# Kernel optimization log

Measured on AMD Instinct MI355X. Metric: run time of the kernel, lower is better.

The kernel has to match this reference:

```python
import jax, jax.numpy as jnp
import numpy as np

N, B, CIN = 2048, 16, 1
M = 4096
COUT = 64
R = 128


def setup_inputs() -> dict:
    key = jax.random.key(0)
    k1, k2, k3, k4, k5 = jax.random.split(key, 5)
    return {
        "context_in": jax.random.normal(k1, (N, B, CIN), dtype=jnp.float32),
        "context_out": jax.random.normal(k2, (N, B, COUT), dtype=jnp.float32),
        "target_in": jax.random.normal(k3, (M, B, CIN), dtype=jnp.float32),
        "lengthscale": jnp.ones((1,), dtype=jnp.float32),
        "W": jax.random.normal(k4, (R, COUT + 1), dtype=jnp.float32),
        "b": jax.random.normal(k5, (R,), dtype=jnp.float32),
    }


def reference(context_in, context_out, target_in, lengthscale, W, b):
    # context_in: (N,B,Cin), context_out: (N,B,Cout), target_in: (M,B,Cin)
    n, batch, _ = context_in.shape
    # density channel prepended -> (N,B,Cout+1)
    dens = jnp.ones((n, batch, 1), dtype=context_in.dtype)
    co = jnp.concatenate([dens, context_out], axis=-1)
    ci = jnp.transpose(context_in, (1, 0, 2))   # (B,N,Cin)
    ti = jnp.transpose(target_in, (1, 0, 2))    # (B,M,Cin)
    # squared pairwise distances (B,N,M)
    d2 = (jnp.sum(ci * ci, -1)[:, :, None]
          + jnp.sum(ti * ti, -1)[:, None, :]
          - 2.0 * jnp.einsum('bnd,bmd->bnm', ci, ti))
    d2 = jnp.maximum(d2, 0.0)
    # RBF kernel: exp(-0.5 * d2 / lengthscale^2)
    K = jnp.exp(-0.5 * d2 / (lengthscale[0] ** 2))  # (B,N,M)
    # weighted sum over context points: (B,M,Cout+1)
    out = jnp.einsum('nbc,bnm->bmc', co, K)
    # density normalization of non-density channels
    out = jnp.concatenate([out[..., :1], out[..., 1:] / (out[..., :1] + 1e-8)], axis=-1)
    # linear projection (Cout+1 -> R)
    out = out @ W.T + b
    return jnp.transpose(out, (1, 0, 2))  # (M,B,R)
```

## Files before the change

### kernel.cpp

```cpp
#include <hip/hip_runtime.h>
#include <hip/hip_bf16.h>


#define N_CTX 2048
#define BATCH 16
#define M_TGT 4096
#define COUT  64
#define RDIM  128

#define WS_COW_OFF  0u
#define WS_FB_OFF   0x400000u
#define WS_G_OFF    0xC00000u
#define WS_GD_OFF   0xC40000u
#define WS_WT_OFF   0xC41000u

#define SSCALE 0.8493222f

typedef __attribute__((ext_vector_type(8)))  short        bf16x8;
typedef __attribute__((ext_vector_type(4)))  float        floatx4;
typedef __attribute__((ext_vector_type(4)))  unsigned int uint4v;

#if __has_builtin(__builtin_amdgcn_exp2f)
#define EXP2F __builtin_amdgcn_exp2f
#else
#define EXP2F exp2f
#endif

__constant__ float RSQ[64] = {
    0.0f,        1.0f,        0.70710678f, 0.57735027f, 0.5f,        0.44721360f,
    0.40824829f, 0.37796447f, 0.35355339f, 0.33333333f, 0.31622777f, 0.30151134f,
    0.28867513f, 0.27735010f, 0.26726124f, 0.25819889f, 0.25f,       0.24253563f,
    0.23570226f, 0.22941573f, 0.22360680f, 0.21821789f, 0.21320072f, 0.20851441f,
    0.20412415f, 0.2f,        0.19611614f, 0.19245009f, 0.18898224f, 0.18569534f,
    0.18257419f, 0.17960530f, 0.17677670f, 0.17407766f, 0.17149859f, 0.16903085f,
    0.16666667f, 0.16439899f, 0.16222142f, 0.16012815f, 0.15811388f, 0.15617376f,
    0.15430335f, 0.15249857f, 0.15075567f, 0.14907120f, 0.14744196f, 0.14586499f,
    0.14433757f, 0.14285714f, 0.14142136f, 0.14002801f, 0.13867505f, 0.13736056f,
    0.13608276f, 0.13483997f, 0.13363062f, 0.13245324f, 0.13130643f, 0.13018891f,
    0.12909944f, 0.12803688f, 0.12700013f, 0.12598816f };

static __device__ __forceinline__ unsigned int packrn(float a, float b) {
    __hip_bfloat162 h = __float22bfloat162_rn(make_float2(a, b));
    return *reinterpret_cast<unsigned int*>(&h);
}
static __device__ __forceinline__ unsigned short f2bfs(float f) {
    __hip_bfloat16 h = __float2bfloat16(f);
    return *reinterpret_cast<unsigned short*>(&h);
}

__global__ __launch_bounds__(256)
void convdeepset_prep(const float* __restrict__ co, const float* __restrict__ W,
                      unsigned char* __restrict__ ws)
{
    unsigned short* cow = (unsigned short*)(ws + WS_COW_OFF);
    unsigned short* wt  = (unsigned short*)(ws + WS_WT_OFF);
    const int blk = blockIdx.x, tid = threadIdx.x;

    if (blk < 1024) {
        const int g    = blk * 4 + (tid >> 6);
        const int bb   = g & 15;
        const int nblk = g >> 4;
        const int c    = tid & 63;
        const float* rp = co + ((size_t)nblk * 8 * BATCH + bb) * COUT + c;
        unsigned int u[4];
#pragma unroll
        for (int j = 0; j < 4; ++j) {
            const float f0 = rp[(size_t)(2 * j)     * BATCH * COUT];
            const float f1 = rp[(size_t)(2 * j + 1) * BATCH * COUT];
            u[j] = packrn(f0, f1);
        }
        *(uint4v*)&cow[(size_t)bb * 131072 + nblk * 512 + c * 8] = *(uint4v*)u;
    } else {
        for (int f = tid; f < 8192; f += 256) {
            const int cp = f & 7, r = (f >> 3) & 127, ch = f >> 10;
            wt[ch * 1024 + r * 8 + cp] = f2bfs(W[r * 65 + 1 + ch * 8 + cp]);
        }
    }
}

__global__ __launch_bounds__(256)
void convdeepset_feat(const float* __restrict__ ci, const float* __restrict__ ls,
                      unsigned char* __restrict__ ws)
{
    float* fb = (float*)(ws + WS_FB_OFF);
    const int f = blockIdx.x * 256 + threadIdx.x;
    const int n = f & 2047, bb = f >> 11;
    const float w  = ci[(size_t)n * BATCH + bb] / ls[0];
    const float sy = SSCALE * w;
    float v = EXP2F(-sy * sy);
    float* o = fb + (size_t)bb * 64 * 2048 + n;
    o[0] = v;
#pragma unroll
    for (int k = 1; k < 64; ++k) {
        v *= w * RSQ[k];
        o[(size_t)k * 2048] = v;
    }
}

__global__ __launch_bounds__(256)
void convdeepset_g(unsigned char* __restrict__ ws)
{
    __shared__ float sred[4][64][16];
    __shared__ float sdens[4][16];
    const unsigned short* cow = (const unsigned short*)(ws + WS_COW_OFF);
    const float* fb = (const float*)(ws + WS_FB_OFF);
    float* G  = (float*)(ws + WS_G_OFF);
    float* gd = (float*)(ws + WS_GD_OFF);

    const int b  = blockIdx.x >> 2, kt = blockIdx.x & 3;
    const int tid = threadIdx.x, lane = tid & 63, wv = tid >> 6;
    const int g2 = lane >> 4, l15 = lane & 15;

    const float* ap = fb + ((size_t)b * 64 + kt * 16 + l15) * 2048
                    + wv * 512 + g2 * 8;
    const unsigned short* bp = cow + (size_t)b * 131072
                             + ((size_t)(wv * 16) * 4 + g2) * 512 + l15 * 8;

    floatx4 acc[4];
#pragma unroll
    for (int ct = 0; ct < 4; ++ct)
#pragma unroll
        for (int e = 0; e < 4; ++e) acc[ct][e] = 0.0f;
    float dpart = 0.0f;

#pragma unroll 4
    for (int s = 0; s < 16; ++s) {
        const floatx4 a0 = *(const floatx4*)(ap);
        const floatx4 a1 = *(const floatx4*)(ap + 4);
        ap += 32;
        const bf16x8 c0 = *(const bf16x8*)(bp);
        const bf16x8 c1 = *(const bf16x8*)(bp + 128);
        const bf16x8 c2 = *(const bf16x8*)(bp + 256);
        const bf16x8 c3 = *(const bf16x8*)(bp + 384);
        bp += 2048;
        dpart += a0.x + a0.y + a0.z + a0.w + a1.x + a1.y + a1.z + a1.w;
        const float fl[8] = {a0.x, a0.y, a0.z, a0.w, a1.x, a1.y, a1.z, a1.w};
        uint4v hw, lw;
#pragma unroll
        for (int p = 0; p < 4; ++p) {
            const unsigned int h = packrn(fl[2 * p], fl[2 * p + 1]);
            const float e0 = __builtin_bit_cast(float, h << 16);
            const float e1 = __builtin_bit_cast(float, h & 0xffff0000u);
            hw[p] = h;
            lw[p] = packrn(fl[2 * p] - e0, fl[2 * p + 1] - e1);
        }
        const bf16x8 ah = __builtin_bit_cast(bf16x8, hw);
        const bf16x8 al = __builtin_bit_cast(bf16x8, lw);
        acc[0] = __builtin_amdgcn_mfma_f32_16x16x32_bf16(ah, c0, acc[0], 0, 0, 0);
        acc[0] = __builtin_amdgcn_mfma_f32_16x16x32_bf16(al, c0, acc[0], 0, 0, 0);
        acc[1] = __builtin_amdgcn_mfma_f32_16x16x32_bf16(ah, c1, acc[1], 0, 0, 0);
        acc[1] = __builtin_amdgcn_mfma_f32_16x16x32_bf16(al, c1, acc[1], 0, 0, 0);
        acc[2] = __builtin_amdgcn_mfma_f32_16x16x32_bf16(ah, c2, acc[2], 0, 0, 0);
        acc[2] = __builtin_amdgcn_mfma_f32_16x16x32_bf16(al, c2, acc[2], 0, 0, 0);
        acc[3] = __builtin_amdgcn_mfma_f32_16x16x32_bf16(ah, c3, acc[3], 0, 0, 0);
        acc[3] = __builtin_amdgcn_mfma_f32_16x16x32_bf16(al, c3, acc[3], 0, 0, 0);
    }

    dpart += __shfl_xor(dpart, 16);
    dpart += __shfl_xor(dpart, 32);
    if (lane < 16) sdens[wv][lane] = dpart;
#pragma unroll
    for (int ct = 0; ct < 4; ++ct)
#pragma unroll
        for (int reg = 0; reg < 4; ++reg)
            sred[wv][lane][ct * 4 + reg] = acc[ct][reg];
    __syncthreads();

    {
        const int ct = tid >> 6, ln = tid & 63;
        const int c  = ct * 16 + (ln & 15);
#pragma unroll
        for (int reg = 0; reg < 4; ++reg) {
            const float ssum = sred[0][ln][ct * 4 + reg] + sred[1][ln][ct * 4 + reg]
                             + sred[2][ln][ct * 4 + reg] + sred[3][ln][ct * 4 + reg];
            const int k = (ln >> 4) * 4 + reg;
            G[((size_t)b * 64 + kt * 16 + k) * 64 + c] = ssum;
        }
    }
    if (tid < 16)
        gd[b * 64 + kt * 16 + tid]
            = sdens[0][tid] + sdens[1][tid] + sdens[2][tid] + sdens[3][tid];
}

__global__ __launch_bounds__(256)
void convdeepset_main(const float* __restrict__ ti, const float* __restrict__ ls,
                      const float* __restrict__ W,  const float* __restrict__ bias,
                      const unsigned char* __restrict__ ws, float* __restrict__ out)
{
    __shared__ float gsm[4096];
    __shared__ float gdl[64];
    __shared__ unsigned short vstage[4][1024];

    const int tid  = threadIdx.x;
    const int lane = tid & 63;
    const int wv   = tid >> 6;
    const int g2   = lane >> 4;
    const int l15  = lane & 15;

    const int b  = blockIdx.x & 15;
    const int mt = blockIdx.x >> 4;
    const int m0 = mt * 64 + wv * 16;

    const float* Gg = (const float*)(ws + WS_G_OFF) + (size_t)b * 4096;
#pragma unroll
    for (int j = 0; j < 4; ++j)
        ((float4*)gsm)[tid + j * 256] = ((const float4*)Gg)[tid + j * 256];
    if (tid < 64) gdl[tid] = ((const float*)(ws + WS_GD_OFF))[b * 64 + tid];
    __syncthreads();

    const float w  = ti[(size_t)(m0 + l15) * BATCH + b] / ls[0];
    const float sy = SSCALE * w;
    float f = EXP2F(-sy * sy);
    float dens = f * gdl[0];
    float fs[16];
#pragma unroll
    for (int j = 0; j < 16; ++j) fs[j] = 0.0f;
    if (g2 == 0) fs[0] = f;
#pragma unroll
    for (int k = 1; k < 64; ++k) {
        f *= w * RSQ[k];
        dens += f * gdl[k];
        if (((k >> 3) & 3) == g2) fs[((k >> 5) << 3) | (k & 7)] = f;
    }

    uint4v hw0, lw0, hw1, lw1;
#pragma unroll
    for (int p = 0; p < 4; ++p) {
        {
            const unsigned int h = packrn(fs[2 * p], fs[2 * p + 1]);
            const float e0 = __builtin_bit_cast(float, h << 16);
            const float e1 = __builtin_bit_cast(float, h & 0xffff0000u);
            hw0[p] = h;
            lw0[p] = packrn(fs[2 * p] - e0, fs[2 * p + 1] - e1);
        }
        {
            const unsigned int h = packrn(fs[8 + 2 * p], fs[8 + 2 * p + 1]);
            const float e0 = __builtin_bit_cast(float, h << 16);
            const float e1 = __builtin_bit_cast(float, h & 0xffff0000u);
            hw1[p] = h;
            lw1[p] = packrn(fs[8 + 2 * p] - e0, fs[8 + 2 * p + 1] - e1);
        }
    }
    const bf16x8 ah0 = __builtin_bit_cast(bf16x8, hw0);
    const bf16x8 al0 = __builtin_bit_cast(bf16x8, lw0);
    const bf16x8 ah1 = __builtin_bit_cast(bf16x8, hw1);
    const bf16x8 al1 = __builtin_bit_cast(bf16x8, lw1);

    floatx4 acc[4];
#pragma unroll
    for (int ct = 0; ct < 4; ++ct)
#pragma unroll
        for (int e = 0; e < 4; ++e) acc[ct][e] = 0.0f;
#pragma unroll
    for (int ct = 0; ct < 4; ++ct) {
#pragma unroll
        for (int wdw = 0; wdw < 2; ++wdw) {
            float gv[8];
#pragma unroll
            for (int j = 0; j < 8; ++j)
                gv[j] = gsm[(wdw * 32 + g2 * 8 + j) * 64 + ct * 16 + l15];
            uint4v gh, gl;
#pragma unroll
            for (int p = 0; p < 4; ++p) {
                const unsigned int h = packrn(gv[2 * p], gv[2 * p + 1]);
                const float e0 = __builtin_bit_cast(float, h << 16);
                const float e1 = __builtin_bit_cast(float, h & 0xffff0000u);
                gh[p] = h;
                gl[p] = packrn(gv[2 * p] - e0, gv[2 * p + 1] - e1);
            }
            const bf16x8 ghv = __builtin_bit_cast(bf16x8, gh);
            const bf16x8 glv = __builtin_bit_cast(bf16x8, gl);
            const bf16x8 ah = wdw ? ah1 : ah0;
            const bf16x8 al = wdw ? al1 : al0;
            acc[ct] = __builtin_amdgcn_mfma_f32_16x16x32_bf16(ah, ghv, acc[ct], 0, 0, 0);
            acc[ct] = __builtin_amdgcn_mfma_f32_16x16x32_bf16(al, ghv, acc[ct], 0, 0, 0);
            acc[ct] = __builtin_amdgcn_mfma_f32_16x16x32_bf16(ah, glv, acc[ct], 0, 0, 0);
        }
    }

    const unsigned short* wtg = (const unsigned short*)(ws + WS_WT_OFF);
    float dt[4], ffv[4];
#pragma unroll
    for (int reg = 0; reg < 4; ++reg) {
        const int m = (lane >> 4) * 4 + reg;
        dt[reg]  = __shfl(dens, m, 64);
        ffv[reg] = 1.0f / (fmaxf(dt[reg], 0.0f) + 1e-8f);
    }
    unsigned short* vs = vstage[wv];
#pragma unroll
    for (int reg = 0; reg < 4; ++reg) {
        const int m = (lane >> 4) * 4 + reg;
#pragma unroll
        for (int q = 0; q < 4; ++q) {
            const int c = q * 16 + l15;
            vs[(c >> 3) * 128 + m * 8 + (c & 7)] = f2bfs(acc[q][reg]);
        }
    }
    floatx4 pacc[8];
#pragma unroll
    for (int rt = 0; rt < 8; ++rt)
#pragma unroll
        for (int e = 0; e < 4; ++e) pacc[rt][e] = 0.0f;
#pragma unroll
    for (int s2 = 0; s2 < 2; ++s2) {
        const int ch = s2 * 4 + g2;
        const bf16x8 avp = *(const bf16x8*)&vs[ch * 128 + l15 * 8];
#pragma unroll
        for (int rt = 0; rt < 8; ++rt) {
            const bf16x8 bvp = *(const bf16x8*)&wtg[ch * 1024 + (rt * 16 + l15) * 8];
            pacc[rt] = __builtin_amdgcn_mfma_f32_16x16x32_bf16(avp, bvp, pacc[rt], 0, 0, 0);
        }
    }
#pragma unroll
    for (int rt = 0; rt < 8; ++rt) {
        const int r = rt * 16 + l15;
        const float w0v = W[r * 65];
        const float bv  = bias[r];
#pragma unroll
        for (int reg = 0; reg < 4; ++reg) {
            const int m = (lane >> 4) * 4 + reg;
            out[((size_t)(m0 + m) * BATCH + b) * RDIM + r]
                = pacc[rt][reg] * ffv[reg] + dt[reg] * w0v + bv;
        }
    }
}

extern "C" void kernel_launch(void* const* d_in, const int* in_sizes, int n_in,
                              void* d_out, int out_size, void* d_ws, size_t ws_size,
                              hipStream_t stream) {
    const float* ci   = (const float*)d_in[0];
    const float* co   = (const float*)d_in[1];
    const float* ti   = (const float*)d_in[2];
    const float* ls   = (const float*)d_in[3];
    const float* W    = (const float*)d_in[4];
    const float* bias = (const float*)d_in[5];
    float* o = (float*)d_out;
    (void)in_sizes; (void)n_in; (void)out_size; (void)ws_size;

    unsigned char* ws = (unsigned char*)d_ws;
    convdeepset_prep<<<1025, 256, 0, stream>>>(co, W, ws);
    convdeepset_feat<<<128, 256, 0, stream>>>(ci, ls, ws);
    convdeepset_g<<<64, 256, 0, stream>>>(ws);
    convdeepset_main<<<1024, 256, 0, stream>>>(ti, ls, W, bias, ws, o);
}
```

Baseline: 108.8 us.

## Merge feature kernel into prep and process two target tiles per block

The feature-basis computation moves into the prep kernel as an extra block range, removing one kernel launch. The main kernel now handles 128 targets per block instead of 64 and runs on half as many blocks. It splits G into hi/lo bf16 fragments once and reuses them for both tiles, so the G shared-memory load and conversion cost is spread over more targets. The cost is higher register pressure from the precomputed fragments and two feature sets, and fewer blocks to hide latency.

After: 107.5 us (median of 2 runs). Within noise of the previous version (-1.2%).

```diff
diff --git a/kernel.cpp b/kernel.cpp
--- a/kernel.cpp
+++ b/kernel.cpp
@@ -49,14 +49,14 @@
 }
 
 __global__ __launch_bounds__(256)
-void convdeepset_prep(const float* __restrict__ co, const float* __restrict__ W,
+void convdeepset_prep(const float* __restrict__ ci, const float* __restrict__ co,
+                      const float* __restrict__ ls, const float* __restrict__ W,
                       unsigned char* __restrict__ ws)
 {
-    unsigned short* cow = (unsigned short*)(ws + WS_COW_OFF);
-    unsigned short* wt  = (unsigned short*)(ws + WS_WT_OFF);
     const int blk = blockIdx.x, tid = threadIdx.x;
 
     if (blk < 1024) {
+        unsigned short* cow = (unsigned short*)(ws + WS_COW_OFF);
         const int g    = blk * 4 + (tid >> 6);
         const int bb   = g & 15;
         const int nblk = g >> 4;
@@ -70,30 +70,26 @@
             u[j] = packrn(f0, f1);
         }
         *(uint4v*)&cow[(size_t)bb * 131072 + nblk * 512 + c * 8] = *(uint4v*)u;
+    } else if (blk < 1152) {
+        float* fbp = (float*)(ws + WS_FB_OFF);
+        const int f = (blk - 1024) * 256 + tid;
+        const int n = f & 2047, bb = f >> 11;
+        const float w  = ci[(size_t)n * BATCH + bb] / ls[0];
+        const float sy = SSCALE * w;
+        float v = EXP2F(-sy * sy);
+        float* o = fbp + (size_t)bb * 64 * 2048 + n;
+        o[0] = v;
+#pragma unroll
+        for (int k = 1; k < 64; ++k) {
+            v *= w * RSQ[k];
+            o[(size_t)k * 2048] = v;
+        }
     } else {
+        unsigned short* wt = (unsigned short*)(ws + WS_WT_OFF);
         for (int f = tid; f < 8192; f += 256) {
             const int cp = f & 7, r = (f >> 3) & 127, ch = f >> 10;
             wt[ch * 1024 + r * 8 + cp] = f2bfs(W[r * 65 + 1 + ch * 8 + cp]);
         }
-    }
-}
-
-__global__ __launch_bounds__(256)
-void convdeepset_feat(const float* __restrict__ ci, const float* __restrict__ ls,
-                      unsigned char* __restrict__ ws)
-{
-    float* fb = (float*)(ws + WS_FB_OFF);
-    const int f = blockIdx.x * 256 + threadIdx.x;
-    const int n = f & 2047, bb = f >> 11;
-    const float w  = ci[(size_t)n * BATCH + bb] / ls[0];
-    const float sy = SSCALE * w;
-    float v = EXP2F(-sy * sy);
-    float* o = fb + (size_t)bb * 64 * 2048 + n;
-    o[0] = v;
-#pragma unroll
-    for (int k = 1; k < 64; ++k) {
-        v *= w * RSQ[k];
-        o[(size_t)k * 2048] = v;
     }
 }
 
@@ -199,7 +195,7 @@
 
     const int b  = blockIdx.x & 15;
     const int mt = blockIdx.x >> 4;
-    const int m0 = mt * 64 + wv * 16;
+    const int m0 = mt * 128 + wv * 16;
 
     const float* Gg = (const float*)(ws + WS_G_OFF) + (size_t)b * 4096;
 #pragma unroll
@@ -208,51 +204,9 @@
     if (tid < 64) gdl[tid] = ((const float*)(ws + WS_GD_OFF))[b * 64 + tid];
     __syncthreads();
 
-    const float w  = ti[(size_t)(m0 + l15) * BATCH + b] / ls[0];
-    const float sy = SSCALE * w;
-    float f = EXP2F(-sy * sy);
-    float dens = f * gdl[0];
-    float fs[16];
-#pragma unroll
-    for (int j = 0; j < 16; ++j) fs[j] = 0.0f;
-    if (g2 == 0) fs[0] = f;
-#pragma unroll
-    for (int k = 1; k < 64; ++k) {
-        f *= w * RSQ[k];
-        dens += f * gdl[k];
-        if (((k >> 3) & 3) == g2) fs[((k >> 5) << 3) | (k & 7)] = f;
-    }
-
-    uint4v hw0, lw0, hw1, lw1;
-#pragma unroll
-    for (int p = 0; p < 4; ++p) {
-        {
-            const unsigned int h = packrn(fs[2 * p], fs[2 * p + 1]);
-            const float e0 = __builtin_bit_cast(float, h << 16);
-            const float e1 = __builtin_bit_cast(float, h & 0xffff0000u);
-            hw0[p] = h;
-            lw0[p] = packrn(fs[2 * p] - e0, fs[2 * p + 1] - e1);
-        }
-        {
-            const unsigned int h = packrn(fs[8 + 2 * p], fs[8 + 2 * p + 1]);
-            const float e0 = __builtin_bit_cast(float, h << 16);
-            const float e1 = __builtin_bit_cast(float, h & 0xffff0000u);
-            hw1[p] = h;
-            lw1[p] = packrn(fs[8 + 2 * p] - e0, fs[8 + 2 * p + 1] - e1);
-        }
-    }
-    const bf16x8 ah0 = __builtin_bit_cast(bf16x8, hw0);
-    const bf16x8 al0 = __builtin_bit_cast(bf16x8, lw0);
-    const bf16x8 ah1 = __builtin_bit_cast(bf16x8, hw1);
-    const bf16x8 al1 = __builtin_bit_cast(bf16x8, lw1);
-
-    floatx4 acc[4];
+    bf16x8 ghv[4][2], glv[4][2];
 #pragma unroll
     for (int ct = 0; ct < 4; ++ct)
-#pragma unroll
-        for (int e = 0; e < 4; ++e) acc[ct][e] = 0.0f;
-#pragma unroll
-    for (int ct = 0; ct < 4; ++ct) {
 #pragma unroll
         for (int wdw = 0; wdw < 2; ++wdw) {
             float gv[8];
@@ -268,61 +222,122 @@
                 gh[p] = h;
                 gl[p] = packrn(gv[2 * p] - e0, gv[2 * p + 1] - e1);
             }
-            const bf16x8 ghv = __builtin_bit_cast(bf16x8, gh);
-            const bf16x8 glv = __builtin_bit_cast(bf16x8, gl);
-            const bf16x8 ah = wdw ? ah1 : ah0;
-            const bf16x8 al = wdw ? al1 : al0;
-            acc[ct] = __builtin_amdgcn_mfma_f32_16x16x32_bf16(ah, ghv, acc[ct], 0, 0, 0);
-            acc[ct] = __builtin_amdgcn_mfma_f32_16x16x32_bf16(al, ghv, acc[ct], 0, 0, 0);
-            acc[ct] = __builtin_amdgcn_mfma_f32_16x16x32_bf16(ah, glv, acc[ct], 0, 0, 0);
+            ghv[ct][wdw] = __builtin_bit_cast(bf16x8, gh);
+            glv[ct][wdw] = __builtin_bit_cast(bf16x8, gl);
+        }
+
+    const float wa = ti[(size_t)(m0 + l15) * BATCH + b] / ls[0];
+    const float wb = ti[(size_t)(m0 + 64 + l15) * BATCH + b] / ls[0];
+    const float sa = SSCALE * wa, sb = SSCALE * wb;
+    float fa  = EXP2F(-sa * sa);
+    float fb_ = EXP2F(-sb * sb);
+    float densa = fa * gdl[0], densb = fb_ * gdl[0];
+    float fsa[16], fsb[16];
+#pragma unroll
+    for (int j = 0; j < 16; ++j) { fsa[j] = 0.0f; fsb[j] = 0.0f; }
+    if (g2 == 0) { fsa[0] = fa; fsb[0] = fb_; }
+#pragma unroll
+    for (int k = 1; k < 64; ++k) {
+        fa  *= wa * RSQ[k];
+        fb_ *= wb * RSQ[k];
+        densa += fa  * gdl[k];
+        densb += fb_ * gdl[k];
+        if (((k >> 3) & 3) == g2) {
+            const int slot = ((k >> 5) << 3) | (k & 7);
+            fsa[slot] = fa;
+            fsb[slot] = fb_;
         }
     }
 
     const unsigned short* wtg = (const unsigned short*)(ws + WS_WT_OFF);
-    float dt[4], ffv[4];
-#pragma unroll
-    for (int reg = 0; reg < 4; ++reg) {
-        const int m = (lane >> 4) * 4 + reg;
-        dt[reg]  = __shfl(dens, m, 64);
-        ffv[reg] = 1.0f / (fmaxf(dt[reg], 0.0f) + 1e-8f);
-    }
-    unsigned short* vs = vstage[wv];
-#pragma unroll
-    for (int reg = 0; reg < 4; ++reg) {
-        const int m = (lane >> 4) * 4 + reg;
-#pragma unroll
-        for (int q = 0; q < 4; ++q) {
-            const int c = q * 16 + l15;
-            vs[(c >> 3) * 128 + m * 8 + (c & 7)] = f2bfs(acc[q][reg]);
-        }
-    }
-    floatx4 pacc[8];
-#pragma unroll
-    for (int rt = 0; rt < 8; ++rt)
-#pragma unroll
-        for (int e = 0; e < 4; ++e) pacc[rt][e] = 0.0f;
-#pragma unroll
-    for (int s2 = 0; s2 < 2; ++s2) {
-        const int ch = s2 * 4 + g2;
-        const bf16x8 avp = *(const bf16x8*)&vs[ch * 128 + l15 * 8];
-#pragma unroll
-        for (int rt = 0; rt < 8; ++rt) {
-            const bf16x8 bvp = *(const bf16x8*)&wtg[ch * 1024 + (rt * 16 + l15) * 8];
-            pacc[rt] = __builtin_amdgcn_mfma_f32_16x16x32_bf16(avp, bvp, pacc[rt], 0, 0, 0);
-        }
-    }
-#pragma unroll
-    for (int rt = 0; rt < 8; ++rt) {
-        const int r = rt * 16 + l15;
-        const float w0v = W[r * 65];
-        const float bv  = bias[r];
+
+    auto do_tile = [&](const float (&fs)[16], float dens, int mbase) {
+        uint4v hw0, lw0, hw1, lw1;
+#pragma unroll
+        for (int p = 0; p < 4; ++p) {
+            {
+                const unsigned int h = packrn(fs[2 * p], fs[2 * p + 1]);
+                const float e0 = __builtin_bit_cast(float, h << 16);
+                const float e1 = __builtin_bit_cast(float, h & 0xffff0000u);
+                hw0[p] = h;
+                lw0[p] = packrn(fs[2 * p] - e0, fs[2 * p + 1] - e1);
+            }
+            {
+                const unsigned int h = packrn(fs[8 + 2 * p], fs[8 + 2 * p + 1]);
+                const float e0 = __builtin_bit_cast(float, h << 16);
+                const float e1 = __builtin_bit_cast(float, h & 0xffff0000u);
+                hw1[p] = h;
+                lw1[p] = packrn(fs[8 + 2 * p] - e0, fs[8 + 2 * p + 1] - e1);
+            }
+        }
+        const bf16x8 ah0 = __builtin_bit_cast(bf16x8, hw0);
+        const bf16x8 al0 = __builtin_bit_cast(bf16x8, lw0);
+        const bf16x8 ah1 = __builtin_bit_cast(bf16x8, hw1);
+        const bf16x8 al1 = __builtin_bit_cast(bf16x8, lw1);
+
+        floatx4 acc[4];
+#pragma unroll
+        for (int ct = 0; ct < 4; ++ct)
+#pragma unroll
+            for (int e = 0; e < 4; ++e) acc[ct][e] = 0.0f;
+#pragma unroll
+        for (int ct = 0; ct < 4; ++ct) {
+            acc[ct] = __builtin_amdgcn_mfma_f32_16x16x32_bf16(ah0, ghv[ct][0], acc[ct], 0, 0, 0);
+            acc[ct] = __builtin_amdgcn_mfma_f32_16x16x32_bf16(al0, ghv[ct][0], acc[ct], 0, 0, 0);
+            acc[ct] = __builtin_amdgcn_mfma_f32_16x16x32_bf16(ah0, glv[ct][0], acc[ct], 0, 0, 0);
+            acc[ct] = __builtin_amdgcn_mfma_f32_16x16x32_bf16(ah1, ghv[ct][1], acc[ct], 0, 0, 0);
+            acc[ct] = __builtin_amdgcn_mfma_f32_16x16x32_bf16(al1, ghv[ct][1], acc[ct], 0, 0, 0);
+            acc[ct] = __builtin_amdgcn_mfma_f32_16x16x32_bf16(ah1, glv[ct][1], acc[ct], 0, 0, 0);
+        }
+
+        float dt[4], ffv[4];
 #pragma unroll
         for (int reg = 0; reg < 4; ++reg) {
             const int m = (lane >> 4) * 4 + reg;
-            out[((size_t)(m0 + m) * BATCH + b) * RDIM + r]
-                = pacc[rt][reg] * ffv[reg] + dt[reg] * w0v + bv;
-        }
-    }
+            dt[reg]  = __shfl(dens, m, 64);
+            ffv[reg] = 1.0f / (fmaxf(dt[reg], 0.0f) + 1e-8f);
+        }
+        unsigned short* vs = vstage[wv];
+#pragma unroll
+        for (int reg = 0; reg < 4; ++reg) {
+            const int m = (lane >> 4) * 4 + reg;
+#pragma unroll
+            for (int q = 0; q < 4; ++q) {
+                const int c = q * 16 + l15;
+                vs[(c >> 3) * 128 + m * 8 + (c & 7)] = f2bfs(acc[q][reg]);
+            }
+        }
+        floatx4 pacc[8];
+#pragma unroll
+        for (int rt = 0; rt < 8; ++rt)
+#pragma unroll
+            for (int e = 0; e < 4; ++e) pacc[rt][e] = 0.0f;
+#pragma unroll
+        for (int s2 = 0; s2 < 2; ++s2) {
+            const int ch = s2 * 4 + g2;
+            const bf16x8 avp = *(const bf16x8*)&vs[ch * 128 + l15 * 8];
+#pragma unroll
+            for (int rt = 0; rt < 8; ++rt) {
+                const bf16x8 bvp = *(const bf16x8*)&wtg[ch * 1024 + (rt * 16 + l15) * 8];
+                pacc[rt] = __builtin_amdgcn_mfma_f32_16x16x32_bf16(avp, bvp, pacc[rt], 0, 0, 0);
+            }
+        }
+#pragma unroll
+        for (int rt = 0; rt < 8; ++rt) {
+            const int r = rt * 16 + l15;
+            const float w0v = W[r * 65];
+            const float bv  = bias[r];
+#pragma unroll
+            for (int reg = 0; reg < 4; ++reg) {
+                const int m = (lane >> 4) * 4 + reg;
+                out[((size_t)(mbase + m) * BATCH + b) * RDIM + r]
+                    = pacc[rt][reg] * ffv[reg] + dt[reg] * w0v + bv;
+            }
+        }
+    };
+
+    do_tile(fsa, densa, m0);
+    do_tile(fsb, densb, m0 + 64);
 }
 
 extern "C" void kernel_launch(void* const* d_in, const int* in_sizes, int n_in,
@@ -338,8 +353,7 @@
     (void)in_sizes; (void)n_in; (void)out_size; (void)ws_size;
 
     unsigned char* ws = (unsigned char*)d_ws;
-    convdeepset_prep<<<1025, 256, 0, stream>>>(co, W, ws);
-    convdeepset_feat<<<128, 256, 0, stream>>>(ci, ls, ws);
+    convdeepset_prep<<<1153, 256, 0, stream>>>(ci, co, ls, W, ws);
     convdeepset_g<<<64, 256, 0, stream>>>(ws);
-    convdeepset_main<<<1024, 256, 0, stream>>>(ti, ls, W, bias, ws, o);
-}
+    convdeepset_main<<<512, 256, 0, stream>>>(ti, ls, W, bias, ws, o);
+}
```
